# Kernel tuning notes

Measured on AMD Instinct MI355X. Metric: run time of the kernel, lower is better.

The kernel has to match this reference:

```python
import jax, jax.numpy as jnp
import numpy as np

N = 50000      # nodes
E = 800000     # edges (before self-loops)
F_IN = 128     # num_features
H = 4          # heads
C = 64         # hidden_channels
HC = H * C     # 256
NEG_SLOPE = 0.2


def setup_inputs() -> dict:
    key = jax.random.key(0)
    ks = jax.random.split(key, 20)
    x = jax.random.normal(ks[0], (N, F_IN), dtype=jnp.float32)
    edge_index = jax.random.randint(ks[1], (2, E), 0, N, dtype=jnp.int32)
    s = 0.05
    inp = {"x": x, "edge_index": edge_index}
    dims_in = [F_IN, HC, HC, HC]
    for l in range(4):
        kW, ka, kb = jax.random.split(ks[2 + l], 3)
        inp[f"W{l+1}"] = jax.random.normal(kW, (dims_in[l], HC), dtype=jnp.float32) * s
        inp[f"a_src{l+1}"] = jax.random.normal(ka, (H, C), dtype=jnp.float32) * s
        inp[f"a_dst{l+1}"] = jax.random.normal(kb, (H, C), dtype=jnp.float32) * s
        inp[f"b{l+1}"] = jnp.zeros((HC,), dtype=jnp.float32)
    return inp


def gat_conv(x, src, dst, W, a_src, a_dst, b):
    # x: [N, F_in] -> h: [N, H, C]
    h = (x @ W).reshape(N, H, C)
    es = jnp.sum(h * a_src, axis=-1)  # [N, H] per-node source logits
    ed = jnp.sum(h * a_dst, axis=-1)  # [N, H]
    e = jax.nn.leaky_relu(es[src] + ed[dst], NEG_SLOPE)  # [Etot, H]
    m = jax.ops.segment_max(e, dst, num_segments=N)      # per-dst max
    m = jnp.where(jnp.isfinite(m), m, 0.0)
    ex = jnp.exp(e - m[dst])
    denom = jax.ops.segment_sum(ex, dst, num_segments=N)
    alpha = ex / (denom[dst] + 1e-16)                     # edge softmax
    out = jax.ops.segment_sum(alpha[:, :, None] * h[src], dst, num_segments=N)
    return out.reshape(N, HC) + b


def reference(x, edge_index,
              W1, a_src1, a_dst1, b1,
              W2, a_src2, a_dst2, b2,
              W3, a_src3, a_dst3, b3,
              W4, a_src4, a_dst4, b4):
    loop = jnp.arange(N, dtype=edge_index.dtype)
    src = jnp.concatenate([edge_index[0], loop])  # add self-loops (PyG default)
    dst = jnp.concatenate([edge_index[1], loop])
    x1 = jax.nn.relu(gat_conv(x, src, dst, W1, a_src1, a_dst1, b1))
    x2 = jax.nn.relu(gat_conv(x1, src, dst, W2, a_src2, a_dst2, b2))
    x3 = jax.nn.relu(gat_conv(x2 + x1, src, dst, W3, a_src3, a_dst3, b3))
    x4 = jax.nn.relu(gat_conv(x2 + x3, src, dst, W4, a_src4, a_dst4, b4))
    # NOTE: source code calls conv4 again (not conv5) -- reproduced faithfully
    x5 = gat_conv(x4 + x3, src, dst, W4, a_src4, a_dst4, b4)
    return x5
```

## Files before the change

kernel.cpp:

```cpp
#include <hip/hip_runtime.h>
#include <hip/hip_bf16.h>

#define N_NODES 50000
#define E_EDGES 800000
#define ETOT (E_EDGES + N_NODES)
#define HC 256
#define NHEAD 4
#define CHAN 64
#define NEG 0.2f
#define NBLK ((N_NODES + 1023) / 1024)

typedef _Float16 half8 __attribute__((ext_vector_type(8)));
typedef _Float16 half4v __attribute__((ext_vector_type(4)));
typedef float float4v __attribute__((ext_vector_type(4)));


__global__ void count_kernel(const int* __restrict__ ei, int* __restrict__ counts) {
    int i = blockIdx.x * blockDim.x + threadIdx.x;
    if (i >= ETOT) return;
    int dst = (i < E_EDGES) ? ei[E_EDGES + i] : (i - E_EDGES);
    atomicAdd(&counts[dst], 1);
}

__global__ __launch_bounds__(256) void blocksum_kernel(const int* __restrict__ counts,
                                                       int* __restrict__ blocksums) {
    __shared__ int s[4];
    int b = blockIdx.x, tid = threadIdx.x;
    int base = b * 1024;
    int sum = 0;
    #pragma unroll
    for (int r = 0; r < 4; ++r) {
        int idx = base + r * 256 + tid;
        sum += (idx < N_NODES) ? counts[idx] : 0;
    }
    #pragma unroll
    for (int m = 1; m < 64; m <<= 1) sum += __shfl_xor(sum, m, 64);
    if ((tid & 63) == 0) s[tid >> 6] = sum;
    __syncthreads();
    if (tid == 0) blocksums[b] = s[0] + s[1] + s[2] + s[3];
}

__global__ __launch_bounds__(64) void blockscan_kernel(int* __restrict__ blocksums) {
    int tid = threadIdx.x;
    int v = (tid < NBLK) ? blocksums[tid] : 0;
    #pragma unroll
    for (int off = 1; off < 64; off <<= 1) {
        int t = __shfl_up(v, off, 64);
        if (tid >= off) v += t;
    }
    if (tid < NBLK) blocksums[tid] = v;
}

__global__ __launch_bounds__(1024) void scatter_scan_kernel(const int* __restrict__ counts,
                                                            const int* __restrict__ blocksums,
                                                            int* __restrict__ offsets,
                                                            int* __restrict__ cursor) {
    __shared__ int s[1024];
    int b = blockIdx.x, tid = threadIdx.x;
    int idx = b * 1024 + tid;
    int v = (idx < N_NODES) ? counts[idx] : 0;
    s[tid] = v;
    __syncthreads();
    for (int off = 1; off < 1024; off <<= 1) {
        int t = (tid >= off) ? s[tid - off] : 0;
        __syncthreads();
        s[tid] += t;
        __syncthreads();
    }
    int excl = s[tid] - v + (b > 0 ? blocksums[b - 1] : 0);
    if (idx < N_NODES) { offsets[idx] = excl; cursor[idx] = excl; }
    if (idx == N_NODES - 1) offsets[N_NODES] = excl + v;
}

__global__ void fill_kernel(const int* __restrict__ ei, int* __restrict__ cursor,
                            int* __restrict__ csr_src, int* __restrict__ csr_dst) {
    int i = blockIdx.x * blockDim.x + threadIdx.x;
    if (i >= ETOT) return;
    int src, dst;
    if (i < E_EDGES) { src = ei[i]; dst = ei[E_EDGES + i]; }
    else             { src = i - E_EDGES; dst = src; }
    int pos = atomicAdd(&cursor[dst], 1);
    csr_src[pos] = src;
    csr_dst[pos] = dst;
}


__global__ void wsplit_kernel(const float* __restrict__ W, _Float16* __restrict__ Wth,
                              _Float16* __restrict__ Wtl, int K) {
    int id = blockIdx.x * 256 + threadIdx.x;
    if (id >= K * 256) return;
    int n = id & 255, k = id >> 8;
    float w = W[(size_t)k * 256 + n];
    _Float16 h = (_Float16)w;
    _Float16 l = (_Float16)(w - (float)h);
    Wth[(size_t)n * K + k] = h;
    Wtl[(size_t)n * K + k] = l;
}

__global__ void xsplit_kernel(const float* __restrict__ x, _Float16* __restrict__ xh,
                              _Float16* __restrict__ xl, int total) {
    int id = blockIdx.x * 256 + threadIdx.x;
    if (id >= total) return;
    float v = x[id];
    _Float16 h = (_Float16)v;
    xh[id] = h;
    xl[id] = (_Float16)(v - (float)h);
}


__global__ __launch_bounds__(256) void edge_alpha_kernel(
        const float* __restrict__ es, const float* __restrict__ ed,
        const int* __restrict__ csr_src, const int* __restrict__ csr_dst,
        float* __restrict__ ex) {
    int e = blockIdx.x * 256 + threadIdx.x;
    if (e >= ETOT) return;
    int s = csr_src[e], d = csr_dst[e];
    float4 esv = *(const float4*)(es + (size_t)s * 4);
    float4 edv = *(const float4*)(ed + (size_t)d * 4);
    float4 v;
    v.x = esv.x + edv.x; v.y = esv.y + edv.y;
    v.z = esv.z + edv.z; v.w = esv.w + edv.w;
    v.x = (v.x > 0.f) ? v.x : NEG * v.x;
    v.y = (v.y > 0.f) ? v.y : NEG * v.y;
    v.z = (v.z > 0.f) ? v.z : NEG * v.z;
    v.w = (v.w > 0.f) ? v.w : NEG * v.w;
    v.x = __expf(v.x); v.y = __expf(v.y);
    v.z = __expf(v.z); v.w = __expf(v.w);
    *(float4*)(ex + (size_t)e * 4) = v;
}


#define LDK 40

__global__ __launch_bounds__(256) void gemm_mfma_kernel(
        const _Float16* __restrict__ A1h, const _Float16* __restrict__ A1l,
        const _Float16* __restrict__ A2h,
        const _Float16* __restrict__ Wth, const _Float16* __restrict__ Wtl,
        const float* __restrict__ a_src, const float* __restrict__ a_dst,
        _Float16* __restrict__ H16, float* __restrict__ es, float* __restrict__ ed,
        int M, int K) {
    __shared__ _Float16 Ah[64][LDK];
    __shared__ _Float16 Al[64][LDK];
    __shared__ _Float16 Bh[256][LDK];
    __shared__ _Float16 Bl[256][LDK];

    int tid = threadIdx.x;
    int m0 = blockIdx.x * 64;
    int w = tid >> 6, lane = tid & 63;
    int rn = w * 64;
    int fr = lane & 15;
    int q  = lane >> 4;
    int fk = q * 8;

    int wr = tid >> 2;
    int wk = (tid & 3) * 8;

    bool has_lo = (A1l != nullptr);
    bool has2   = (A2h != nullptr);

    float4v acc[4][4];
    #pragma unroll
    for (int i = 0; i < 4; ++i)
        #pragma unroll
        for (int j = 0; j < 4; ++j)
            acc[i][j] = (float4v){0.f, 0.f, 0.f, 0.f};

    half8 pa, pal, pbh[4], pbl[4];

    auto load_tile = [&](int k0) {
        int row = m0 + wr;
        pa  = (half8)(_Float16)0;
        pal = (half8)(_Float16)0;
        if (row < M) {
            pa = *(const half8*)(A1h + (size_t)row * K + k0 + wk);
            if (has2) {
                half8 u = *(const half8*)(A2h + (size_t)row * K + k0 + wk);
                pa = pa + u;
            }
            if (has_lo) pal = *(const half8*)(A1l + (size_t)row * K + k0 + wk);
        }
        #pragma unroll
        for (int g = 0; g < 4; ++g) {
            int r = g * 64 + wr;
            pbh[g] = *(const half8*)(Wth + (size_t)r * K + k0 + wk);
            pbl[g] = *(const half8*)(Wtl + (size_t)r * K + k0 + wk);
        }
    };

    load_tile(0);
    for (int k0 = 0; k0 < K; k0 += 32) {
        *(half8*)&Ah[wr][wk] = pa;
        if (has_lo) *(half8*)&Al[wr][wk] = pal;
        #pragma unroll
        for (int g = 0; g < 4; ++g) {
            int r = g * 64 + wr;
            *(half8*)&Bh[r][wk] = pbh[g];
            *(half8*)&Bl[r][wk] = pbl[g];
        }
        __syncthreads();
        if (k0 + 32 < K) load_tile(k0 + 32);
        half8 afh[4], bfh[4], bfl[4];
        #pragma unroll
        for (int t = 0; t < 4; ++t) {
            afh[t] = *(const half8*)&Ah[t * 16 + fr][fk];
            bfh[t] = *(const half8*)&Bh[rn + t * 16 + fr][fk];
            bfl[t] = *(const half8*)&Bl[rn + t * 16 + fr][fk];
        }
        if (has_lo) {
            half8 afl[4];
            #pragma unroll
            for (int t = 0; t < 4; ++t) afl[t] = *(const half8*)&Al[t * 16 + fr][fk];
            #pragma unroll
            for (int tm = 0; tm < 4; ++tm)
                #pragma unroll
                for (int tn = 0; tn < 4; ++tn)
                    acc[tm][tn] = __builtin_amdgcn_mfma_f32_16x16x32_f16(
                        afl[tm], bfh[tn], acc[tm][tn], 0, 0, 0);
        }
        #pragma unroll
        for (int tm = 0; tm < 4; ++tm)
            #pragma unroll
            for (int tn = 0; tn < 4; ++tn) {
                float4v c = acc[tm][tn];
                c = __builtin_amdgcn_mfma_f32_16x16x32_f16(afh[tm], bfl[tn], c, 0, 0, 0);
                c = __builtin_amdgcn_mfma_f32_16x16x32_f16(afh[tm], bfh[tn], c, 0, 0, 0);
                acc[tm][tn] = c;
            }
        __syncthreads();
    }

    float asv[4], adv[4];
    #pragma unroll
    for (int tn = 0; tn < 4; ++tn) {
        asv[tn] = a_src[w * CHAN + tn * 16 + fr];
        adv[tn] = a_dst[w * CHAN + tn * 16 + fr];
    }
    #pragma unroll
    for (int tm = 0; tm < 4; ++tm) {
        #pragma unroll
        for (int i = 0; i < 4; ++i) {
            int row = m0 + tm * 16 + q * 4 + i;
            float ps = 0.f, pd = 0.f;
            #pragma unroll
            for (int tn = 0; tn < 4; ++tn) {
                float hv = acc[tm][tn][i];
                ps += hv * asv[tn];
                pd += hv * adv[tn];
                if (row < M)
                    H16[(size_t)row * HC + rn + tn * 16 + fr] = (_Float16)hv;
            }
            #pragma unroll
            for (int msk = 1; msk < 16; msk <<= 1) {
                ps += __shfl_xor(ps, msk, 64);
                pd += __shfl_xor(pd, msk, 64);
            }
            if (fr == 0 && row < M) {
                es[row * NHEAD + w] = ps;
                ed[row * NHEAD + w] = pd;
            }
        }
    }
}


__global__ __launch_bounds__(256) void gat_aggregate_kernel(
        const _Float16* __restrict__ H16, const float* __restrict__ ex,
        const int* __restrict__ offsets, const int* __restrict__ csr_src,
        const float* __restrict__ bias, _Float16* __restrict__ out16,
        float* __restrict__ out32, int do_relu) {
    __shared__ float ex_lds[4][256];
    __shared__ int   src_lds[4][64];
    int tid = threadIdx.x;
    int w = tid >> 6, lane = tid & 63;
    int n = blockIdx.x * 4 + w;
    int off = offsets[n];
    int deg = offsets[n + 1] - off;

    if (deg <= 64) {
        int sreg = n;
        float4 ex4 = make_float4(0.f, 0.f, 0.f, 0.f);
        if (lane < deg) {
            sreg = csr_src[off + lane];
            ex4 = *(const float4*)(ex + (size_t)(off + lane) * 4);
        }
        src_lds[w][lane] = sreg;
        *(float4*)&ex_lds[w][lane * 4] = ex4;

        int hl = lane & 31, side = lane >> 5;
        int hd = hl >> 3;
        float av[8] = {0.f, 0.f, 0.f, 0.f, 0.f, 0.f, 0.f, 0.f};
        int degr = (deg + 7) & ~7;
        #pragma unroll 2
        for (int j0 = 0; j0 < degr; j0 += 8) {
            int j = j0 + side;
            int s0 = src_lds[w][j];
            int s1 = src_lds[w][j + 2];
            int s2 = src_lds[w][j + 4];
            int s3 = src_lds[w][j + 6];
            float w0 = ex_lds[w][j * 4 + hd];
            float w1 = ex_lds[w][(j + 2) * 4 + hd];
            float w2 = ex_lds[w][(j + 4) * 4 + hd];
            float w3 = ex_lds[w][(j + 6) * 4 + hd];
            half8 h0 = *(const half8*)(H16 + (size_t)s0 * HC + hl * 8);
            half8 h1 = *(const half8*)(H16 + (size_t)s1 * HC + hl * 8);
            half8 h2 = *(const half8*)(H16 + (size_t)s2 * HC + hl * 8);
            half8 h3 = *(const half8*)(H16 + (size_t)s3 * HC + hl * 8);
            #pragma unroll
            for (int c = 0; c < 8; ++c) {
                av[c] += w0 * (float)h0[c];
                av[c] += w1 * (float)h1[c];
                av[c] += w2 * (float)h2[c];
                av[c] += w3 * (float)h3[c];
            }
        }

        float4 l4 = ex4;
        #pragma unroll
        for (int msk = 1; msk < 64; msk <<= 1) {
            l4.x += __shfl_xor(l4.x, msk, 64);
            l4.y += __shfl_xor(l4.y, msk, 64);
            l4.z += __shfl_xor(l4.z, msk, 64);
            l4.w += __shfl_xor(l4.w, msk, 64);
        }
        #pragma unroll
        for (int c = 0; c < 8; ++c) av[c] += __shfl_xor(av[c], 32, 64);
        if (side == 0) {
            float denom = (hd == 0) ? l4.x : (hd == 1) ? l4.y : (hd == 2) ? l4.z : l4.w;
            float scale = 1.f / (denom + 1e-16f);
            float4 b0 = *(const float4*)(bias + hl * 8);
            float4 b1 = *(const float4*)(bias + hl * 8 + 4);
            float o[8] = {av[0] * scale + b0.x, av[1] * scale + b0.y,
                          av[2] * scale + b0.z, av[3] * scale + b0.w,
                          av[4] * scale + b1.x, av[5] * scale + b1.y,
                          av[6] * scale + b1.z, av[7] * scale + b1.w};
            if (do_relu)
                #pragma unroll
                for (int c = 0; c < 8; ++c) o[c] = fmaxf(o[c], 0.f);
            if (out16) {
                half8 ov = {(_Float16)o[0], (_Float16)o[1], (_Float16)o[2], (_Float16)o[3],
                            (_Float16)o[4], (_Float16)o[5], (_Float16)o[6], (_Float16)o[7]};
                *(half8*)(out16 + (size_t)n * HC + hl * 8) = ov;
            } else {
                *(float4*)(out32 + (size_t)n * HC + hl * 8) =
                    make_float4(o[0], o[1], o[2], o[3]);
                *(float4*)(out32 + (size_t)n * HC + hl * 8 + 4) =
                    make_float4(o[4], o[5], o[6], o[7]);
            }
        }
        return;
    }

    int head = lane >> 4;
    float4 acc0 = make_float4(0.f, 0.f, 0.f, 0.f);
    float den = 0.f;
    for (int j = 0; j < deg; ++j) {
        int s = csr_src[off + j];
        float exv = ex[(size_t)(off + j) * 4 + head];
        den += exv;
        half4v h0 = *(const half4v*)(H16 + (size_t)s * HC + lane * 4);
        acc0.x += exv * (float)h0[0]; acc0.y += exv * (float)h0[1];
        acc0.z += exv * (float)h0[2]; acc0.w += exv * (float)h0[3];
    }
    float scale = 1.f / (den + 1e-16f);
    float4 b4 = *(const float4*)(bias + lane * 4);
    float o[4] = {acc0.x * scale + b4.x, acc0.y * scale + b4.y,
                  acc0.z * scale + b4.z, acc0.w * scale + b4.w};
    if (do_relu)
        #pragma unroll
        for (int c = 0; c < 4; ++c) o[c] = fmaxf(o[c], 0.f);
    if (out16) {
        half4v ov = {(_Float16)o[0], (_Float16)o[1], (_Float16)o[2], (_Float16)o[3]};
        *(half4v*)(out16 + (size_t)n * HC + lane * 4) = ov;
    } else {
        *(float4*)(out32 + (size_t)n * HC + lane * 4) = make_float4(o[0], o[1], o[2], o[3]);
    }
}


extern "C" void kernel_launch(void* const* d_in, const int* in_sizes, int n_in,
                              void* d_out, int out_size, void* d_ws, size_t ws_size,
                              hipStream_t stream) {
    const float* x  = (const float*)d_in[0];
    const int*   ei = (const int*)d_in[1];
    const float *W[5], *Asrc[5], *Adst[5], *Bs[5];
    for (int l = 0; l < 4; ++l) {
        W[l]    = (const float*)d_in[2 + l * 4];
        Asrc[l] = (const float*)d_in[3 + l * 4];
        Adst[l] = (const float*)d_in[4 + l * 4];
        Bs[l]   = (const float*)d_in[5 + l * 4];
    }
    W[4] = W[3]; Asrc[4] = Asrc[3]; Adst[4] = Adst[3]; Bs[4] = Bs[3];

    char* ws = (char*)d_ws;
    size_t off = 0;
    auto alloc = [&](size_t bytes) -> void* {
        void* p = ws + off;
        off += (bytes + 255) & ~(size_t)255;
        return p;
    };
    _Float16* h16  = (_Float16*)alloc((size_t)N_NODES * HC * 2);
    _Float16* xa   = (_Float16*)alloc((size_t)N_NODES * HC * 2);
    _Float16* xb   = (_Float16*)alloc((size_t)N_NODES * HC * 2);
    _Float16* xc   = (_Float16*)alloc((size_t)N_NODES * HC * 2);
    _Float16* xd   = (_Float16*)alloc((size_t)N_NODES * HC * 2);
    _Float16* xh   = (_Float16*)alloc((size_t)N_NODES * 128 * 2);
    _Float16* xl   = (_Float16*)alloc((size_t)N_NODES * 128 * 2);
    float* es      = (float*)alloc((size_t)N_NODES * 4 * 4);
    float* ed      = (float*)alloc((size_t)N_NODES * 4 * 4);
    float* exbuf   = (float*)alloc((size_t)ETOT * 4 * 4);
    int*   counts  = (int*)alloc((size_t)N_NODES * 4);
    int*   offsets = (int*)alloc((size_t)(N_NODES + 1) * 4);
    int*   cursor  = (int*)alloc((size_t)N_NODES * 4);
    int*   csr_src = (int*)alloc((size_t)ETOT * 4);
    int*   csr_dst = (int*)alloc((size_t)ETOT * 4);
    int*   blocksums = (int*)alloc((size_t)NBLK * 4);
    _Float16 *Wth[5], *Wtl[5];
    int Ks[4] = {128, 256, 256, 256};
    for (int l = 0; l < 4; ++l) {
        Wth[l] = (_Float16*)alloc((size_t)256 * Ks[l] * 2);
        Wtl[l] = (_Float16*)alloc((size_t)256 * Ks[l] * 2);
    }
    Wth[4] = Wth[3]; Wtl[4] = Wtl[3];

    hipMemsetAsync(counts, 0, (size_t)N_NODES * 4, stream);
    count_kernel<<<(ETOT + 255) / 256, 256, 0, stream>>>(ei, counts);
    blocksum_kernel<<<NBLK, 256, 0, stream>>>(counts, blocksums);
    blockscan_kernel<<<1, 64, 0, stream>>>(blocksums);
    scatter_scan_kernel<<<NBLK, 1024, 0, stream>>>(counts, blocksums, offsets, cursor);
    fill_kernel<<<(ETOT + 255) / 256, 256, 0, stream>>>(ei, cursor, csr_src, csr_dst);
    for (int l = 0; l < 4; ++l)
        wsplit_kernel<<<(Ks[l] * 256 + 255) / 256, 256, 0, stream>>>(W[l], Wth[l], Wtl[l], Ks[l]);
    xsplit_kernel<<<(N_NODES * 128 + 255) / 256, 256, 0, stream>>>(x, xh, xl, N_NODES * 128);

    auto layer = [&](const _Float16* a1h, const _Float16* a1l, const _Float16* a2h,
                     int K, int l, _Float16* o16, float* o32, int relu) {
        gemm_mfma_kernel<<<(N_NODES + 63) / 64, 256, 0, stream>>>(
            a1h, a1l, a2h, Wth[l], Wtl[l], Asrc[l], Adst[l], h16, es, ed, N_NODES, K);
        edge_alpha_kernel<<<(ETOT + 255) / 256, 256, 0, stream>>>(
            es, ed, csr_src, csr_dst, exbuf);
        gat_aggregate_kernel<<<N_NODES / 4, 256, 0, stream>>>(
            h16, exbuf, offsets, csr_src, Bs[l], o16, o32, relu);
    };

    float* out = (float*)d_out;
    layer(xh, xl,      nullptr, 128, 0, xa, nullptr, 1);
    layer(xa, nullptr, nullptr, 256, 1, xb, nullptr, 1);
    layer(xb, nullptr, xa,      256, 2, xc, nullptr, 1);
    layer(xb, nullptr, xc,      256, 3, xd, nullptr, 1);
    layer(xd, nullptr, xc,      256, 4, nullptr, out, 0);
}
```

Measured before the change: 749.2 us.

## Template GEMM on K and flags; stage full A row-block in LDS upfront

```diff
diff --git a/kernel.cpp b/kernel.cpp
--- a/kernel.cpp
+++ b/kernel.cpp
@@ -130,19 +130,21 @@
 }
 
 
-#define LDK 40
-
+template<int K, bool HASLO, bool HAS2>
 __global__ __launch_bounds__(256) void gemm_mfma_kernel(
         const _Float16* __restrict__ A1h, const _Float16* __restrict__ A1l,
         const _Float16* __restrict__ A2h,
         const _Float16* __restrict__ Wth, const _Float16* __restrict__ Wtl,
         const float* __restrict__ a_src, const float* __restrict__ a_dst,
         _Float16* __restrict__ H16, float* __restrict__ es, float* __restrict__ ed,
-        int M, int K) {
-    __shared__ _Float16 Ah[64][LDK];
-    __shared__ _Float16 Al[64][LDK];
-    __shared__ _Float16 Bh[256][LDK];
-    __shared__ _Float16 Bl[256][LDK];
+        int M) {
+    constexpr int LDA = K + 16;
+    constexpr int NC  = K / 32;
+    constexpr int CPR = K / 8;
+    __shared__ _Float16 Ah[64][LDA];
+    __shared__ _Float16 Al[HASLO ? 64 : 1][HASLO ? LDA : 8];
+    __shared__ _Float16 Bh[256][40];
+    __shared__ _Float16 Bl[256][40];
 
     int tid = threadIdx.x;
     int m0 = blockIdx.x * 64;
@@ -155,30 +157,25 @@
     int wr = tid >> 2;
     int wk = (tid & 3) * 8;
 
-    bool has_lo = (A1l != nullptr);
-    bool has2   = (A2h != nullptr);
-
-    float4v acc[4][4];
-    #pragma unroll
-    for (int i = 0; i < 4; ++i)
-        #pragma unroll
-        for (int j = 0; j < 4; ++j)
-            acc[i][j] = (float4v){0.f, 0.f, 0.f, 0.f};
-
-    half8 pa, pal, pbh[4], pbl[4];
-
-    auto load_tile = [&](int k0) {
-        int row = m0 + wr;
-        pa  = (half8)(_Float16)0;
-        pal = (half8)(_Float16)0;
-        if (row < M) {
-            pa = *(const half8*)(A1h + (size_t)row * K + k0 + wk);
-            if (has2) {
-                half8 u = *(const half8*)(A2h + (size_t)row * K + k0 + wk);
-                pa = pa + u;
-            }
-            if (has_lo) pal = *(const half8*)(A1l + (size_t)row * K + k0 + wk);
-        }
+    half8 a1c[NC], a2c[HAS2 ? NC : 1], alc[HASLO ? NC : 1];
+    #pragma unroll
+    for (int c = 0; c < NC; ++c) {
+        int idx = c * 256 + tid;
+        int row = idx / CPR, col = (idx % CPR) * 8;
+        int grow = m0 + row;
+        a1c[c] = (half8)(_Float16)0;
+        if (grow < M) a1c[c] = *(const half8*)(A1h + (size_t)grow * K + col);
+        if constexpr (HAS2) {
+            a2c[c] = (half8)(_Float16)0;
+            if (grow < M) a2c[c] = *(const half8*)(A2h + (size_t)grow * K + col);
+        }
+        if constexpr (HASLO) {
+            alc[c] = (half8)(_Float16)0;
+            if (grow < M) alc[c] = *(const half8*)(A1l + (size_t)grow * K + col);
+        }
+    }
+    half8 pbh[4], pbl[4];
+    auto loadB = [&](int k0) {
         #pragma unroll
         for (int g = 0; g < 4; ++g) {
             int r = g * 64 + wr;
@@ -186,11 +183,29 @@
             pbl[g] = *(const half8*)(Wtl + (size_t)r * K + k0 + wk);
         }
     };
-
-    load_tile(0);
-    for (int k0 = 0; k0 < K; k0 += 32) {
-        *(half8*)&Ah[wr][wk] = pa;
-        if (has_lo) *(half8*)&Al[wr][wk] = pal;
+    loadB(0);
+
+    #pragma unroll
+    for (int c = 0; c < NC; ++c) {
+        int idx = c * 256 + tid;
+        int row = idx / CPR, col = (idx % CPR) * 8;
+        half8 v = a1c[c];
+        if constexpr (HAS2) v = v + a2c[c];
+        *(half8*)&Ah[row][col] = v;
+        if constexpr (HASLO) *(half8*)&Al[row][col] = alc[c];
+    }
+
+    float4v acc[4][4];
+    #pragma unroll
+    for (int i = 0; i < 4; ++i)
+        #pragma unroll
+        for (int j = 0; j < 4; ++j)
+            acc[i][j] = (float4v){0.f, 0.f, 0.f, 0.f};
+
+    __syncthreads();
+
+    for (int kk = 0; kk < K / 32; ++kk) {
+        int k0 = kk * 32;
         #pragma unroll
         for (int g = 0; g < 4; ++g) {
             int r = g * 64 + wr;
@@ -198,18 +213,18 @@
             *(half8*)&Bl[r][wk] = pbl[g];
         }
         __syncthreads();
-        if (k0 + 32 < K) load_tile(k0 + 32);
+        if (kk + 1 < K / 32) loadB(k0 + 32);
         half8 afh[4], bfh[4], bfl[4];
         #pragma unroll
         for (int t = 0; t < 4; ++t) {
-            afh[t] = *(const half8*)&Ah[t * 16 + fr][fk];
+            afh[t] = *(const half8*)&Ah[t * 16 + fr][k0 + fk];
             bfh[t] = *(const half8*)&Bh[rn + t * 16 + fr][fk];
             bfl[t] = *(const half8*)&Bl[rn + t * 16 + fr][fk];
         }
-        if (has_lo) {
+        if constexpr (HASLO) {
             half8 afl[4];
             #pragma unroll
-            for (int t = 0; t < 4; ++t) afl[t] = *(const half8*)&Al[t * 16 + fr][fk];
+            for (int t = 0; t < 4; ++t) afl[t] = *(const half8*)&Al[t * 16 + fr][k0 + fk];
             #pragma unroll
             for (int tm = 0; tm < 4; ++tm)
                 #pragma unroll
@@ -432,10 +447,8 @@
         wsplit_kernel<<<(Ks[l] * 256 + 255) / 256, 256, 0, stream>>>(W[l], Wth[l], Wtl[l], Ks[l]);
     xsplit_kernel<<<(N_NODES * 128 + 255) / 256, 256, 0, stream>>>(x, xh, xl, N_NODES * 128);
 
-    auto layer = [&](const _Float16* a1h, const _Float16* a1l, const _Float16* a2h,
-                     int K, int l, _Float16* o16, float* o32, int relu) {
-        gemm_mfma_kernel<<<(N_NODES + 63) / 64, 256, 0, stream>>>(
-            a1h, a1l, a2h, Wth[l], Wtl[l], Asrc[l], Adst[l], h16, es, ed, N_NODES, K);
+    int gemm_grid = (N_NODES + 63) / 64;
+    auto agg = [&](int l, _Float16* o16, float* o32, int relu) {
         edge_alpha_kernel<<<(ETOT + 255) / 256, 256, 0, stream>>>(
             es, ed, csr_src, csr_dst, exbuf);
         gat_aggregate_kernel<<<N_NODES / 4, 256, 0, stream>>>(
@@ -443,9 +456,19 @@
     };
 
     float* out = (float*)d_out;
-    layer(xh, xl,      nullptr, 128, 0, xa, nullptr, 1);
-    layer(xa, nullptr, nullptr, 256, 1, xb, nullptr, 1);
-    layer(xb, nullptr, xa,      256, 2, xc, nullptr, 1);
-    layer(xb, nullptr, xc,      256, 3, xd, nullptr, 1);
-    layer(xd, nullptr, xc,      256, 4, nullptr, out, 0);
-}
+    gemm_mfma_kernel<128, true, false><<<gemm_grid, 256, 0, stream>>>(
+        xh, xl, nullptr, Wth[0], Wtl[0], Asrc[0], Adst[0], h16, es, ed, N_NODES);
+    agg(0, xa, nullptr, 1);
+    gemm_mfma_kernel<256, false, false><<<gemm_grid, 256, 0, stream>>>(
+        xa, nullptr, nullptr, Wth[1], Wtl[1], Asrc[1], Adst[1], h16, es, ed, N_NODES);
+    agg(1, xb, nullptr, 1);
+    gemm_mfma_kernel<256, false, true><<<gemm_grid, 256, 0, stream>>>(
+        xb, nullptr, xa, Wth[2], Wtl[2], Asrc[2], Adst[2], h16, es, ed, N_NODES);
+    agg(2, xc, nullptr, 1);
+    gemm_mfma_kernel<256, false, true><<<gemm_grid, 256, 0, stream>>>(
+        xb, nullptr, xc, Wth[3], Wtl[3], Asrc[3], Adst[3], h16, es, ed, N_NODES);
+    agg(3, xd, nullptr, 1);
+    gemm_mfma_kernel<256, false, true><<<gemm_grid, 256, 0, stream>>>(
+        xd, nullptr, xc, Wth[4], Wtl[4], Asrc[4], Adst[4], h16, es, ed, N_NODES);
+    agg(4, nullptr, out, 0);
+}
```

Result: no change. 753.6 us (+0.6%).
